# Kernel optimization log

Measured on AMD Instinct MI355X. Metric: run time of the kernel, lower is better.

The kernel has to match this reference:

```python
import jax, jax.numpy as jnp
import numpy as np

B, T, D, HS = 32, 2048, 384, 64

def setup_inputs() -> dict:
    key = jax.random.key(0)
    kx, kq, kk, kv = jax.random.split(key, 4)
    x = jax.random.normal(kx, (B, T, D), dtype=jnp.float32)
    s = 1.0 / np.sqrt(D)  # Linear-like init scale
    Wq = jax.random.normal(kq, (D, HS), dtype=jnp.float32) * s
    Wk = jax.random.normal(kk, (D, HS), dtype=jnp.float32) * s
    Wv = jax.random.normal(kv, (D, HS), dtype=jnp.float32) * s
    return {"x": x, "Wq": Wq, "Wk": Wk, "Wv": Wv}

def reference(x, Wq, Wk, Wv):
    # Single-head causal self-attention (dropout in eval mode -> identity).
    Tlen = x.shape[1]
    q = x @ Wq  # [B,T,HS]
    k = x @ Wk
    v = x @ Wv
    scale = q.shape[-1] ** (-0.5)
    wei = jnp.einsum('bqd,bkd->bqk', q, k) * scale  # [B,T,T]
    causal = jnp.tril(jnp.ones((Tlen, Tlen), dtype=bool))
    wei = jnp.where(causal, wei, jnp.finfo(wei.dtype).min)
    wei = jax.nn.softmax(wei, axis=-1)
    return jnp.einsum('bqk,bkd->bqd', wei, v)  # [B,T,HS]
```

## Files before the change

### kernel.cpp

```cpp
#include <hip/hip_runtime.h>
#include <hip/hip_bf16.h>

#define T_LEN 2048
#define NBATCH 32

typedef __bf16 bf16x8 __attribute__((ext_vector_type(8)));
typedef float f32x4 __attribute__((ext_vector_type(4)));

__device__ __forceinline__ unsigned short f2bf(float f) {
  return __builtin_bit_cast(unsigned short, __float2bfloat16(f));
}
__device__ __forceinline__ unsigned int pk2(float a, float b) {
  return (unsigned int)f2bf(a) | ((unsigned int)f2bf(b) << 16);
}
__device__ __forceinline__ unsigned int f2bf_tr(float f) {
  return __builtin_bit_cast(unsigned int, f) >> 16;
}
__device__ __forceinline__ bf16x8 ld16(const void* p) {
  return __builtin_bit_cast(bf16x8, *(const uint4*)p);
}
__device__ __forceinline__ void gl_lds16(const void* g, void* l) {
  __builtin_amdgcn_global_load_lds(
      (const __attribute__((address_space(1))) unsigned int*)g,
      (__attribute__((address_space(3))) unsigned int*)l, 16, 0, 0);
}
__device__ __forceinline__ void bar_raw() {
  asm volatile("s_barrier" ::: "memory");
}

__global__ __launch_bounds__(256) void k_wprep(const float* __restrict__ Wq,
                                               const float* __restrict__ Wk,
                                               const float* __restrict__ Wv,
                                               unsigned short* __restrict__ Wt3) {
  int idx = blockIdx.x * 256 + threadIdx.x;
  if (idx >= 192 * 384) return;
  int c = idx / 384;
  int k = idx % 384;
  const float* W = (c < 64) ? Wq : ((c < 128) ? Wk : Wv);
  Wt3[idx] = f2bf(W[k * 64 + (c & 63)]);
}

__global__ __launch_bounds__(256) void k_proj(const float* __restrict__ x,
                                              const unsigned short* __restrict__ Wt3,
                                              unsigned short* __restrict__ Qb,
                                              unsigned short* __restrict__ Kb,
                                              unsigned short* __restrict__ VTb) {
  __shared__ __align__(16) unsigned short xs[128 * 32];
  __shared__ __align__(16) unsigned short wt[192 * 32];
  const int tid = threadIdx.x;
  const int lane = tid & 63, w = tid >> 6;
  const int g = lane >> 4, lr = lane & 15;
  const long row0 = (long)blockIdx.x * 128;

  f32x4 acc[2][12] = {};

  for (int ks = 0; ks < 12; ++ks) {
    const int k0 = ks * 32;
    __syncthreads();
    {
      int r = tid >> 1, c0 = (tid & 1) * 16;
      const float4* src = reinterpret_cast<const float4*>(&x[(row0 + r) * 384 + k0 + c0]);
      float4 f0 = src[0], f1 = src[1], f2 = src[2], f3 = src[3];
      uint4 u0, u1;
      u0.x = pk2(f0.x, f0.y); u0.y = pk2(f0.z, f0.w);
      u0.z = pk2(f1.x, f1.y); u0.w = pk2(f1.z, f1.w);
      u1.x = pk2(f2.x, f2.y); u1.y = pk2(f2.z, f2.w);
      u1.z = pk2(f3.x, f3.y); u1.w = pk2(f3.z, f3.w);
      int b0 = (r * 64 + c0 * 2) ^ ((r & 7) << 4);
      int b1 = (r * 64 + c0 * 2 + 16) ^ ((r & 7) << 4);
      *reinterpret_cast<uint4*>((char*)xs + b0) = u0;
      *reinterpret_cast<uint4*>((char*)xs + b1) = u1;
    }
#pragma unroll
    for (int j = 0; j < 3; ++j) {
      int chunk = tid + 256 * j;
      int r = chunk >> 2, c8 = chunk & 3;
      uint4 d = *reinterpret_cast<const uint4*>(&Wt3[r * 384 + k0 + c8 * 8]);
      int b = (r * 64 + c8 * 16) ^ ((r & 7) << 4);
      *reinterpret_cast<uint4*>((char*)wt + b) = d;
    }
    __syncthreads();

    bf16x8 a[2];
#pragma unroll
    for (int mt = 0; mt < 2; ++mt) {
      int r = w * 32 + mt * 16 + lr;
      a[mt] = ld16((char*)xs + ((r * 64 + g * 16) ^ ((r & 7) << 4)));
    }
#pragma unroll
    for (int n = 0; n < 12; ++n) {
      int r = n * 16 + lr;
      bf16x8 bb = ld16((char*)wt + ((r * 64 + g * 16) ^ ((r & 7) << 4)));
      acc[0][n] = __builtin_amdgcn_mfma_f32_16x16x32_bf16(a[0], bb, acc[0][n], 0, 0, 0);
      acc[1][n] = __builtin_amdgcn_mfma_f32_16x16x32_bf16(a[1], bb, acc[1][n], 0, 0, 0);
    }
  }

#pragma unroll
  for (int mt = 0; mt < 2; ++mt)
#pragma unroll
    for (int n = 0; n < 12; ++n)
#pragma unroll
      for (int rr = 0; rr < 4; ++rr) {
        long grow = row0 + w * 32 + mt * 16 + g * 4 + rr;
        int col = n * 16 + lr;
        unsigned short hv = f2bf(acc[mt][n][rr]);
        if (n < 4) {
          Qb[grow * 64 + col] = hv;
        } else if (n < 8) {
          Kb[grow * 64 + (col - 64)] = hv;
        } else {
          long bb_ = grow >> 11;
          long t = grow & 2047;
          VTb[(bb_ * 64 + (col - 128)) * 2048 + t] = hv;
        }
      }
}

__global__ __launch_bounds__(512) void k_attn(const unsigned short* __restrict__ Qb,
                                              const unsigned short* __restrict__ Kb,
                                              const unsigned short* __restrict__ VTb,
                                              float* __restrict__ out) {
  __shared__ __align__(16) char ksm[2 * 8192];
  __shared__ __align__(16) char vsm[2 * 8192];
  __shared__ __align__(16) char psm[8 * 2048];

  const int tid = threadIdx.x;
  const int lane = tid & 63, w = tid >> 6;
  const int g = lane >> 4, lr = lane & 15;
  const int b = blockIdx.x;
  const int qt = (gridDim.y - 1) - blockIdx.y;
  const int qrow0 = qt * 128 + w * 16;

  const char* Kg = (const char*)(Kb + (long)b * T_LEN * 64);
  const char* Vg = (const char*)(VTb + (long)b * 64 * 2048);

  const int lrow = lane >> 3;
  const int lsw = (((lane & 7) ^ lrow) << 4);

  bf16x8 qf[2];
#pragma unroll
  for (int c = 0; c < 2; ++c)
    qf[c] = ld16(&Qb[((long)(b * T_LEN + qrow0 + lr)) * 64 + c * 32 + g * 8]);

  f32x4 o[4] = {};
  float m2[4], l_r[4];
#pragma unroll
  for (int r = 0; r < 4; ++r) { m2[r] = -1e30f; l_r[r] = 0.f; }

  const float C2 = 0.125f * 1.44269504f;
  char* pbase = psm + w * 2048;
  const int nkv = 2 * qt + 2;

  gl_lds16(Kg + (long)(w * 8 + lrow) * 128 + lsw, ksm + w * 1024);
  gl_lds16(Vg + (long)(w * 8 + lrow) * 4096 + lsw, vsm + w * 1024);

  int cur = 0;
  for (int t = 0; t < nkv; ++t) {
    const int kv0 = t * 64;

    bar_raw();

    if (t + 1 < nkv) {
      const int kv1 = kv0 + 64;
      gl_lds16(Kg + (long)(kv1 + w * 8 + lrow) * 128 + lsw,
               ksm + (cur ^ 1) * 8192 + w * 1024);
      gl_lds16(Vg + (long)(w * 8 + lrow) * 4096 + (long)kv1 * 2 + lsw,
               vsm + (cur ^ 1) * 8192 + w * 1024);
      asm volatile("s_waitcnt vmcnt(2)" ::: "memory");
    } else {
      asm volatile("s_waitcnt vmcnt(0)" ::: "memory");
    }
    bar_raw();

    if (kv0 <= qrow0 + 15) {
      char* kt = ksm + cur * 8192;
      char* vt = vsm + cur * 8192;

      f32x4 s[4] = {};
      __builtin_amdgcn_s_setprio(1);
#pragma unroll
      for (int c = 0; c < 2; ++c)
#pragma unroll
        for (int n = 0; n < 4; ++n) {
          int r = n * 16 + lr;
          bf16x8 kf = ld16(kt + ((r * 128 + c * 64 + g * 16) ^ ((r & 7) << 4)));
          s[n] = __builtin_amdgcn_mfma_f32_16x16x32_bf16(qf[c], kf, s[n], 0, 0, 0);
        }
      __builtin_amdgcn_s_setprio(0);

      if (kv0 + 63 > qrow0) {
#pragma unroll
        for (int n = 0; n < 4; ++n)
#pragma unroll
          for (int r = 0; r < 4; ++r) {
            int col = kv0 + n * 16 + lr;
            int rowq = qrow0 + g * 4 + r;
            if (col > rowq) s[n][r] = -1e30f;
          }
      }

      float pm[4];
#pragma unroll
      for (int r = 0; r < 4; ++r)
        pm[r] = fmaxf(fmaxf(s[0][r], s[1][r]), fmaxf(s[2][r], s[3][r]));
      bool need = false;
#pragma unroll
      for (int r = 0; r < 4; ++r) need = need || (pm[r] * C2 > m2[r] + 11.5f);
      if (__any((int)need)) {
#pragma unroll
        for (int r = 0; r < 4; ++r) {
          float mx = pm[r];
          mx = fmaxf(mx, __shfl_xor(mx, 1));
          mx = fmaxf(mx, __shfl_xor(mx, 2));
          mx = fmaxf(mx, __shfl_xor(mx, 4));
          mx = fmaxf(mx, __shfl_xor(mx, 8));
          float mn = fmaxf(m2[r], mx * C2);
          float sc = exp2f(m2[r] - mn);
          m2[r] = mn;
          l_r[r] *= sc;
#pragma unroll
          for (int n = 0; n < 4; ++n) o[n][r] *= sc;
        }
      }
      float pr[4][4];
#pragma unroll
      for (int r = 0; r < 4; ++r)
#pragma unroll
        for (int n = 0; n < 4; ++n) {
          float pv = exp2f(__builtin_fmaf(s[n][r], C2, -m2[r]));
          pr[n][r] = pv;
          l_r[r] += pv;
        }

#pragma unroll
      for (int n = 0; n < 4; ++n)
#pragma unroll
        for (int r = 0; r < 4; ++r) {
          int rq = g * 4 + r;
          int col = n * 16 + lr;
          *(unsigned short*)(pbase + ((rq * 128 + col * 2) ^ ((rq & 7) << 4))) =
              (unsigned short)f2bf_tr(pr[n][r]);
        }

      bf16x8 pf[2];
#pragma unroll
      for (int c = 0; c < 2; ++c)
        pf[c] = ld16(pbase + ((lr * 128 + c * 64 + g * 16) ^ ((lr & 7) << 4)));
      __builtin_amdgcn_s_setprio(1);
#pragma unroll
      for (int c = 0; c < 2; ++c)
#pragma unroll
        for (int n = 0; n < 4; ++n) {
          int r = n * 16 + lr;
          bf16x8 vf = ld16(vt + ((r * 128 + c * 64 + g * 16) ^ ((r & 7) << 4)));
          o[n] = __builtin_amdgcn_mfma_f32_16x16x32_bf16(pf[c], vf, o[n], 0, 0, 0);
        }
      __builtin_amdgcn_s_setprio(0);
    }

    cur ^= 1;
  }

#pragma unroll
  for (int r = 0; r < 4; ++r) {
    float l = l_r[r];
    l += __shfl_xor(l, 1);
    l += __shfl_xor(l, 2);
    l += __shfl_xor(l, 4);
    l += __shfl_xor(l, 8);
    float inv = 1.0f / l;
#pragma unroll
    for (int n = 0; n < 4; ++n) {
      long rowg = (long)b * T_LEN + qrow0 + g * 4 + r;
      out[rowg * 64 + n * 16 + lr] = o[n][r] * inv;
    }
  }
}

extern "C" void kernel_launch(void* const* d_in, const int* in_sizes, int n_in,
                              void* d_out, int out_size, void* d_ws, size_t ws_size,
                              hipStream_t stream) {
  const float* x  = (const float*)d_in[0];
  const float* Wq = (const float*)d_in[1];
  const float* Wk = (const float*)d_in[2];
  const float* Wv = (const float*)d_in[3];
  float* out = (float*)d_out;

  char* ws = (char*)d_ws;
  unsigned short* Wt3 = (unsigned short*)ws;
  unsigned short* Qb  = (unsigned short*)(ws + 0x80000);
  unsigned short* Kb  = (unsigned short*)(ws + 0x80000 + 0x800000);
  unsigned short* VTb = (unsigned short*)(ws + 0x80000 + 0x1000000);

  k_wprep<<<dim3(288), dim3(256), 0, stream>>>(Wq, Wk, Wv, Wt3);
  k_proj<<<dim3(512), dim3(256), 0, stream>>>(x, Wt3, Qb, Kb, VTb);
  k_attn<<<dim3(NBATCH, 16), dim3(512), 0, stream>>>(Qb, Kb, VTb, out);
}
```

Baseline: 90.68 us.

## Have each attention wave process 32 query rows with 256-thread blocks

Halves the attention block to 4 waves, each now owning two 16-row query fragments. Every K/V fragment read from LDS then feeds two MFMAs instead of one, and each wave loads twice as much of the K/V tile per stage. The aim is to cut LDS read traffic and barrier overhead per unit of work. In exchange, register pressure roughly doubles and there are fewer waves per block for latency hiding. The causal skip condition also becomes coarser per wave.

```diff
diff --git a/kernel.cpp b/kernel.cpp
--- a/kernel.cpp
+++ b/kernel.cpp
@@ -117,20 +117,20 @@
       }
 }
 
-__global__ __launch_bounds__(512) void k_attn(const unsigned short* __restrict__ Qb,
+__global__ __launch_bounds__(256) void k_attn(const unsigned short* __restrict__ Qb,
                                               const unsigned short* __restrict__ Kb,
                                               const unsigned short* __restrict__ VTb,
                                               float* __restrict__ out) {
   __shared__ __align__(16) char ksm[2 * 8192];
   __shared__ __align__(16) char vsm[2 * 8192];
-  __shared__ __align__(16) char psm[8 * 2048];
+  __shared__ __align__(16) char psm[4 * 4096];
 
   const int tid = threadIdx.x;
   const int lane = tid & 63, w = tid >> 6;
   const int g = lane >> 4, lr = lane & 15;
   const int b = blockIdx.x;
   const int qt = (gridDim.y - 1) - blockIdx.y;
-  const int qrow0 = qt * 128 + w * 16;
+  const int qrow0 = qt * 128 + w * 32;
 
   const char* Kg = (const char*)(Kb + (long)b * T_LEN * 64);
   const char* Vg = (const char*)(VTb + (long)b * 64 * 2048);
@@ -138,22 +138,30 @@
   const int lrow = lane >> 3;
   const int lsw = (((lane & 7) ^ lrow) << 4);
 
-  bf16x8 qf[2];
-#pragma unroll
-  for (int c = 0; c < 2; ++c)
-    qf[c] = ld16(&Qb[((long)(b * T_LEN + qrow0 + lr)) * 64 + c * 32 + g * 8]);
-
-  f32x4 o[4] = {};
-  float m2[4], l_r[4];
-#pragma unroll
-  for (int r = 0; r < 4; ++r) { m2[r] = -1e30f; l_r[r] = 0.f; }
+  bf16x8 qf[2][2];
+#pragma unroll
+  for (int f = 0; f < 2; ++f)
+#pragma unroll
+    for (int c = 0; c < 2; ++c)
+      qf[f][c] = ld16(&Qb[((long)(b * T_LEN + qrow0 + f * 16 + lr)) * 64 + c * 32 + g * 8]);
+
+  f32x4 o[2][4] = {};
+  float m2[2][4], l_r[2][4];
+#pragma unroll
+  for (int f = 0; f < 2; ++f)
+#pragma unroll
+    for (int r = 0; r < 4; ++r) { m2[f][r] = -1e30f; l_r[f][r] = 0.f; }
 
   const float C2 = 0.125f * 1.44269504f;
-  char* pbase = psm + w * 2048;
+  char* pbase = psm + w * 4096;
   const int nkv = 2 * qt + 2;
 
-  gl_lds16(Kg + (long)(w * 8 + lrow) * 128 + lsw, ksm + w * 1024);
-  gl_lds16(Vg + (long)(w * 8 + lrow) * 4096 + lsw, vsm + w * 1024);
+  {
+    const char* gk = Kg + (long)(w * 16 + lrow) * 128 + lsw;
+    const char* gv = Vg + (long)(w * 16 + lrow) * 4096 + lsw;
+    gl_lds16(gk, ksm + w * 2048);             gl_lds16(gk + 8 * 128, ksm + w * 2048 + 1024);
+    gl_lds16(gv, vsm + w * 2048);             gl_lds16(gv + 8 * 4096, vsm + w * 2048 + 1024);
+  }
 
   int cur = 0;
   for (int t = 0; t < nkv; ++t) {
@@ -163,21 +171,23 @@
 
     if (t + 1 < nkv) {
       const int kv1 = kv0 + 64;
-      gl_lds16(Kg + (long)(kv1 + w * 8 + lrow) * 128 + lsw,
-               ksm + (cur ^ 1) * 8192 + w * 1024);
-      gl_lds16(Vg + (long)(w * 8 + lrow) * 4096 + (long)kv1 * 2 + lsw,
-               vsm + (cur ^ 1) * 8192 + w * 1024);
-      asm volatile("s_waitcnt vmcnt(2)" ::: "memory");
+      const char* gk = Kg + (long)(kv1 + w * 16 + lrow) * 128 + lsw;
+      const char* gv = Vg + (long)(w * 16 + lrow) * 4096 + (long)kv1 * 2 + lsw;
+      char* kb = ksm + (cur ^ 1) * 8192 + w * 2048;
+      char* vb = vsm + (cur ^ 1) * 8192 + w * 2048;
+      gl_lds16(gk, kb);           gl_lds16(gk + 8 * 128, kb + 1024);
+      gl_lds16(gv, vb);           gl_lds16(gv + 8 * 4096, vb + 1024);
+      asm volatile("s_waitcnt vmcnt(4)" ::: "memory");
     } else {
       asm volatile("s_waitcnt vmcnt(0)" ::: "memory");
     }
     bar_raw();
 
-    if (kv0 <= qrow0 + 15) {
+    if (kv0 <= qrow0) {
       char* kt = ksm + cur * 8192;
       char* vt = vsm + cur * 8192;
 
-      f32x4 s[4] = {};
+      f32x4 s[2][4] = {};
       __builtin_amdgcn_s_setprio(1);
 #pragma unroll
       for (int c = 0; c < 2; ++c)
@@ -185,68 +195,76 @@
         for (int n = 0; n < 4; ++n) {
           int r = n * 16 + lr;
           bf16x8 kf = ld16(kt + ((r * 128 + c * 64 + g * 16) ^ ((r & 7) << 4)));
-          s[n] = __builtin_amdgcn_mfma_f32_16x16x32_bf16(qf[c], kf, s[n], 0, 0, 0);
+          s[0][n] = __builtin_amdgcn_mfma_f32_16x16x32_bf16(qf[0][c], kf, s[0][n], 0, 0, 0);
+          s[1][n] = __builtin_amdgcn_mfma_f32_16x16x32_bf16(qf[1][c], kf, s[1][n], 0, 0, 0);
         }
       __builtin_amdgcn_s_setprio(0);
 
       if (kv0 + 63 > qrow0) {
 #pragma unroll
+        for (int f = 0; f < 2; ++f)
+#pragma unroll
+          for (int n = 0; n < 4; ++n)
+#pragma unroll
+            for (int r = 0; r < 4; ++r) {
+              int col = kv0 + n * 16 + lr;
+              int rowq = qrow0 + f * 16 + g * 4 + r;
+              if (col > rowq) s[f][n][r] = -1e30f;
+            }
+      }
+
+#pragma unroll
+      for (int f = 0; f < 2; ++f) {
+        float pm[4];
+#pragma unroll
+        for (int r = 0; r < 4; ++r)
+          pm[r] = fmaxf(fmaxf(s[f][0][r], s[f][1][r]), fmaxf(s[f][2][r], s[f][3][r]));
+        bool need = false;
+#pragma unroll
+        for (int r = 0; r < 4; ++r) need = need || (pm[r] * C2 > m2[f][r] + 11.5f);
+        if (__any((int)need)) {
+#pragma unroll
+          for (int r = 0; r < 4; ++r) {
+            float mx = pm[r];
+            mx = fmaxf(mx, __shfl_xor(mx, 1));
+            mx = fmaxf(mx, __shfl_xor(mx, 2));
+            mx = fmaxf(mx, __shfl_xor(mx, 4));
+            mx = fmaxf(mx, __shfl_xor(mx, 8));
+            float mn = fmaxf(m2[f][r], mx * C2);
+            float sc = exp2f(m2[f][r] - mn);
+            m2[f][r] = mn;
+            l_r[f][r] *= sc;
+#pragma unroll
+            for (int n = 0; n < 4; ++n) o[f][n][r] *= sc;
+          }
+        }
+#pragma unroll
         for (int n = 0; n < 4; ++n)
 #pragma unroll
           for (int r = 0; r < 4; ++r) {
-            int col = kv0 + n * 16 + lr;
-            int rowq = qrow0 + g * 4 + r;
-            if (col > rowq) s[n][r] = -1e30f;
+            float pv = exp2f(__builtin_fmaf(s[f][n][r], C2, -m2[f][r]));
+            s[f][n][r] = pv;
+            l_r[f][r] += pv;
+          }
+
+        char* pb = pbase + f * 2048;
+#pragma unroll
+        for (int n = 0; n < 4; ++n)
+#pragma unroll
+          for (int r = 0; r < 4; ++r) {
+            int rq = g * 4 + r;
+            int col = n * 16 + lr;
+            *(unsigned short*)(pb + ((rq * 128 + col * 2) ^ ((rq & 7) << 4))) =
+                (unsigned short)f2bf_tr(s[f][n][r]);
           }
       }
 
-      float pm[4];
-#pragma unroll
-      for (int r = 0; r < 4; ++r)
-        pm[r] = fmaxf(fmaxf(s[0][r], s[1][r]), fmaxf(s[2][r], s[3][r]));
-      bool need = false;
-#pragma unroll
-      for (int r = 0; r < 4; ++r) need = need || (pm[r] * C2 > m2[r] + 11.5f);
-      if (__any((int)need)) {
-#pragma unroll
-        for (int r = 0; r < 4; ++r) {
-          float mx = pm[r];
-          mx = fmaxf(mx, __shfl_xor(mx, 1));
-          mx = fmaxf(mx, __shfl_xor(mx, 2));
-          mx = fmaxf(mx, __shfl_xor(mx, 4));
-          mx = fmaxf(mx, __shfl_xor(mx, 8));
-          float mn = fmaxf(m2[r], mx * C2);
-          float sc = exp2f(m2[r] - mn);
-          m2[r] = mn;
-          l_r[r] *= sc;
-#pragma unroll
-          for (int n = 0; n < 4; ++n) o[n][r] *= sc;
-        }
-      }
-      float pr[4][4];
-#pragma unroll
-      for (int r = 0; r < 4; ++r)
-#pragma unroll
-        for (int n = 0; n < 4; ++n) {
-          float pv = exp2f(__builtin_fmaf(s[n][r], C2, -m2[r]));
-          pr[n][r] = pv;
-          l_r[r] += pv;
-        }
-
-#pragma unroll
-      for (int n = 0; n < 4; ++n)
-#pragma unroll
-        for (int r = 0; r < 4; ++r) {
-          int rq = g * 4 + r;
-          int col = n * 16 + lr;
-          *(unsigned short*)(pbase + ((rq * 128 + col * 2) ^ ((rq & 7) << 4))) =
-              (unsigned short)f2bf_tr(pr[n][r]);
-        }
-
-      bf16x8 pf[2];
-#pragma unroll
-      for (int c = 0; c < 2; ++c)
-        pf[c] = ld16(pbase + ((lr * 128 + c * 64 + g * 16) ^ ((lr & 7) << 4)));
+      bf16x8 pf[2][2];
+#pragma unroll
+      for (int f = 0; f < 2; ++f)
+#pragma unroll
+        for (int c = 0; c < 2; ++c)
+          pf[f][c] = ld16(pbase + f * 2048 + ((lr * 128 + c * 64 + g * 16) ^ ((lr & 7) << 4)));
       __builtin_amdgcn_s_setprio(1);
 #pragma unroll
       for (int c = 0; c < 2; ++c)
@@ -254,7 +272,8 @@
         for (int n = 0; n < 4; ++n) {
           int r = n * 16 + lr;
           bf16x8 vf = ld16(vt + ((r * 128 + c * 64 + g * 16) ^ ((r & 7) << 4)));
-          o[n] = __builtin_amdgcn_mfma_f32_16x16x32_bf16(pf[c], vf, o[n], 0, 0, 0);
+          o[0][n] = __builtin_amdgcn_mfma_f32_16x16x32_bf16(pf[0][c], vf, o[0][n], 0, 0, 0);
+          o[1][n] = __builtin_amdgcn_mfma_f32_16x16x32_bf16(pf[1][c], vf, o[1][n], 0, 0, 0);
         }
       __builtin_amdgcn_s_setprio(0);
     }
@@ -263,19 +282,21 @@
   }
 
 #pragma unroll
-  for (int r = 0; r < 4; ++r) {
-    float l = l_r[r];
-    l += __shfl_xor(l, 1);
-    l += __shfl_xor(l, 2);
-    l += __shfl_xor(l, 4);
-    l += __shfl_xor(l, 8);
-    float inv = 1.0f / l;
-#pragma unroll
-    for (int n = 0; n < 4; ++n) {
-      long rowg = (long)b * T_LEN + qrow0 + g * 4 + r;
-      out[rowg * 64 + n * 16 + lr] = o[n][r] * inv;
-    }
-  }
+  for (int f = 0; f < 2; ++f)
+#pragma unroll
+    for (int r = 0; r < 4; ++r) {
+      float l = l_r[f][r];
+      l += __shfl_xor(l, 1);
+      l += __shfl_xor(l, 2);
+      l += __shfl_xor(l, 4);
+      l += __shfl_xor(l, 8);
+      float inv = 1.0f / l;
+#pragma unroll
+      for (int n = 0; n < 4; ++n) {
+        long rowg = (long)b * T_LEN + qrow0 + f * 16 + g * 4 + r;
+        out[rowg * 64 + n * 16 + lr] = o[f][n][r] * inv;
+      }
+    }
 }
 
 extern "C" void kernel_launch(void* const* d_in, const int* in_sizes, int n_in,
@@ -295,5 +316,5 @@
 
   k_wprep<<<dim3(288), dim3(256), 0, stream>>>(Wq, Wk, Wv, Wt3);
   k_proj<<<dim3(512), dim3(256), 0, stream>>>(x, Wt3, Qb, Kb, VTb);
-  k_attn<<<dim3(NBATCH, 16), dim3(512), 0, stream>>>(Qb, Kb, VTb, out);
-}
+  k_attn<<<dim3(NBATCH, 16), dim3(256), 0, stream>>>(Qb, Kb, VTb, out);
+}
```

Result: slower. 108.9 us (+20.1%).
